# Optimization experiments

Measured on AMD Instinct MI355X. Metric: run time of the kernel, lower is better.

## Reference

```python
import jax, jax.numpy as jnp
import numpy as np

T = 8192        # total tokens
HID = 2048      # hidden_size
H = 16          # num heads
D = 128         # head_dim
INNER = H * D   # 2048
CHUNK = 128
EPS = 1e-5
SCALE = D ** -0.5
ROPE_BASE = 600000.0


def _rmsnorm(x, w, eps=EPS):
    # x: [..., d]
    var = jnp.mean(jnp.square(x), axis=-1, keepdims=True)
    return x * jax.lax.rsqrt(var + eps) * w


def _rope(x, positions):
    # neox-style rope on full head_dim. x: [T, H, D], positions: [T]
    half = D // 2
    inv_freq = 1.0 / (ROPE_BASE ** (jnp.arange(half, dtype=jnp.float32) / half))
    ang = positions.astype(jnp.float32)[:, None] * inv_freq          # [T, half]
    cos = jnp.cos(ang)[:, None, :]                                   # [T, 1, half]
    sin = jnp.sin(ang)[:, None, :]
    x1, x2 = x[..., :half], x[..., half:]
    return jnp.concatenate([x1 * cos - x2 * sin, x2 * cos + x1 * sin], axis=-1)


def setup_inputs() -> dict:
    key = jax.random.key(0)
    ks = jax.random.split(key, 5)
    hidden_states = jax.random.normal(ks[0], (T, HID), dtype=jnp.float32)
    positions = jnp.arange(T, dtype=jnp.int64 if jax.config.jax_enable_x64 else jnp.int32)
    Wqkv = jax.random.normal(ks[1], (HID, 3 * INNER), dtype=jnp.float32) * 0.02
    q_ln_w = jnp.ones((D,), dtype=jnp.float32)
    k_ln_w = jnp.ones((D,), dtype=jnp.float32)
    Wg = jax.random.normal(ks[2], (HID, INNER), dtype=jnp.float32) * 0.02
    g_norm_w = jnp.ones((INNER,), dtype=jnp.float32)
    Wo = jax.random.normal(ks[3], (INNER, HID), dtype=jnp.float32) * 0.02
    return {"hidden_states": hidden_states, "positions": positions, "Wqkv": Wqkv,
            "q_ln_w": q_ln_w, "k_ln_w": k_ln_w, "Wg": Wg,
            "g_norm_w": g_norm_w, "Wo": Wo}


def reference(hidden_states, positions, Wqkv, q_ln_w, k_ln_w, Wg, g_norm_w, Wo):
    x = hidden_states.astype(jnp.float32)
    qkv = jax.nn.silu(x @ Wqkv)                                  # linear_silu=True, fp32
    q, k, v = jnp.split(qkv, [INNER, 2 * INNER], axis=-1)
    # per-head QK RMSNorm
    q = _rmsnorm(q.reshape(T, H, D), q_ln_w)
    k = _rmsnorm(k.reshape(T, H, D), k_ln_w)
    # rope
    q = _rope(q, positions)
    k = _rope(k, positions)
    v = v.reshape(T, H, D)
    q = q * SCALE  # scaling passed to RadixAttention

    # chunked causal linear attention: o_t = q_t @ sum_{s<=t} k_s v_s^T
    N = T // CHUNK
    qc = q.reshape(N, CHUNK, H, D)
    kc = k.reshape(N, CHUNK, H, D)
    vc = v.reshape(N, CHUNK, H, D)
    mask = jnp.tril(jnp.ones((CHUNK, CHUNK), dtype=jnp.float32))  # causal within chunk

    def step(S, chunk):
        qi, ki, vi = chunk                                        # [C, H, D]
        scores = jnp.einsum('chd,shd->hcs', qi, ki) * mask        # intra-chunk causal
        o = jnp.einsum('hcs,shd->chd', scores, vi)
        o = o + jnp.einsum('chd,hde->che', qi, S)                 # inter-chunk state
        S = S + jnp.einsum('chd,che->hde', ki, vi)
        return S, o

    S0 = jnp.zeros((H, D, D), dtype=jnp.float32)
    _, o = jax.lax.scan(step, S0, (qc, kc, vc))                   # o: [N, C, H, D]
    o = o.reshape(T, INNER)

    gate = x @ Wg                                                 # g_proj
    normed = _rmsnorm(o, g_norm_w)                                # group_norm_size == 1
    gated = jax.nn.sigmoid(gate) * normed
    return gated @ Wo                                             # out proj (no bias)
```

## Files before the change

### kernel.cpp

```cpp
#include <hip/hip_runtime.h>
#include <cstdint>
#include <cstddef>

typedef unsigned short u16;
typedef __attribute__((ext_vector_type(8))) short short8;
typedef __attribute__((ext_vector_type(4))) float f32x4;

#define T_SEQ 8192
#define NH 16
#define HD 128
#define NCH 64
#define KDIM 2048

constexpr float EPS = 1e-5f;
constexpr float SCALE = 0.08838834764831845f;

__device__ __forceinline__ u16 f2bf(float f) {
  union { float f; unsigned u; } v; v.f = f;
  unsigned r = v.u + 0x7fffu + ((v.u >> 16) & 1u);
  return (u16)(r >> 16);
}
__device__ __forceinline__ float bf2f(u16 h) {
  union { unsigned u; float f; } v; v.u = ((unsigned)h) << 16;
  return v.f;
}
__device__ __forceinline__ unsigned pack2(u16 a, u16 b) {
  return (unsigned)a | ((unsigned)b << 16);
}
__device__ __forceinline__ f32x4 mfma16(short8 a, short8 b, f32x4 c) {
  return __builtin_amdgcn_mfma_f32_16x16x32_bf16(a, b, c, 0, 0, 0);
}
__device__ __forceinline__ void gl2lds(const u16* g, u16* l) {
  __builtin_amdgcn_global_load_lds(
      (const __attribute__((address_space(1))) void*)g,
      (__attribute__((address_space(3))) void*)l, 16, 0, 0);
}

__global__ __launch_bounds__(256) void cast_f32_bf16(const float* __restrict__ src,
                                                     u16* __restrict__ dst, long n) {
  long i = ((long)blockIdx.x * 256 + threadIdx.x) * 8;
  if (i >= n) return;
  float4 a = *(const float4*)(src + i);
  float4 b = *(const float4*)(src + i + 4);
  alignas(16) u16 u[8] = {f2bf(a.x), f2bf(a.y), f2bf(a.z), f2bf(a.w),
                          f2bf(b.x), f2bf(b.y), f2bf(b.z), f2bf(b.w)};
  *(int4*)(dst + i) = *(const int4*)u;
}

__global__ __launch_bounds__(256) void transpose_cast(const float* __restrict__ W,
                                                      u16* __restrict__ Wt, int K, int N) {
  __shared__ u16 tile[64][72];
  int n0 = blockIdx.x * 64, k0 = blockIdx.y * 64;
  int tx = threadIdx.x, ty = threadIdx.y;
  for (int r = ty; r < 64; r += 4)
    tile[r][tx] = f2bf(W[(size_t)(k0 + r) * N + n0 + tx]);
  __syncthreads();
  for (int r = ty; r < 64; r += 4)
    Wt[(size_t)(n0 + r) * K + k0 + tx] = tile[tx][r];
}

template <int EPI>
__global__ __launch_bounds__(512) void gemm256(const u16* __restrict__ A,
                                               const u16* __restrict__ Bt, int N,
                                               float* __restrict__ Cf,
                                               u16* __restrict__ Cb,
                                               u16* __restrict__ q_t,
                                               u16* __restrict__ k_t,
                                               u16* __restrict__ v_t) {
  __shared__ u16 lds[65536];
  const int tid  = threadIdx.x;
  const int wave = tid >> 6, lane = tid & 63;
  const int lr = lane & 15, lg = lane >> 4;
  const int wr = wave >> 2, wc = wave & 3;
  const int nx = gridDim.x;
  const int nwg = nx * gridDim.y;
  const int flat = blockIdx.y * nx + blockIdx.x;
  const int logical = (flat & 7) * (nwg >> 3) + (flat >> 3);
  const int bm = logical / nx, bn = logical % nx;
  const int sx  = (lr & 7) << 4;
  const int cu0 = ((lg * 16) ^ sx) >> 1;
  const int cu1 = ((64 + lg * 16) ^ sx) >> 1;

  const int srow  = tid >> 3;
  const int sslot = (tid & 7) ^ (srow & 7);
  const u16* gA = A  + (size_t)(bm * 256 + srow) * KDIM + sslot * 8;
  const u16* gB = Bt + (size_t)(bn * 256 + srow) * KDIM + sslot * 8;
  const int sbase = wave * 512;

  f32x4 acc[8][4];
  #pragma unroll
  for (int i = 0; i < 8; i++)
    #pragma unroll
    for (int j = 0; j < 4; j++) acc[i][j] = (f32x4){0.f, 0.f, 0.f, 0.f};

  auto STAGE = [&](int op, int buf, int half, int kt) {
    const u16* g = (op ? gB : gA) + (size_t)half * 128 * KDIM + kt * 64;
    u16* l = &lds[buf * 32768 + op * 16384 + half * 8192 + sbase];
    gl2lds(g, l);
    gl2lds(g + (size_t)64 * KDIM, l + 4096);
  };

  const int aoff = (wr * 64 + lr) * 64;
  const int boff = 16384 + (wc * 32 + lr) * 64;

  STAGE(0, 0, 0, 0); STAGE(1, 0, 0, 0); STAGE(0, 0, 1, 0); STAGE(1, 0, 1, 0);
  STAGE(0, 1, 0, 1); STAGE(1, 1, 1, 1); STAGE(0, 1, 1, 1);
  asm volatile("s_waitcnt vmcnt(6)" ::: "memory");
  __builtin_amdgcn_s_barrier();

  short8 af[4][2], b0f[2][2], b1f[2][2];
  const int NT = KDIM / 64;
  for (int t = 0; t < NT; ++t) {
    const int cur = t & 1, nxt = cur ^ 1;
    const int cb = cur * 32768;
    #pragma unroll
    for (int i = 0; i < 4; i++) {
      af[i][0] = *(const short8*)&lds[cb + aoff + i * 1024 + cu0];
      af[i][1] = *(const short8*)&lds[cb + aoff + i * 1024 + cu1];
    }
    #pragma unroll
    for (int j = 0; j < 2; j++) {
      b0f[j][0] = *(const short8*)&lds[cb + boff + j * 1024 + cu0];
      b0f[j][1] = *(const short8*)&lds[cb + boff + j * 1024 + cu1];
    }
    if (t + 1 < NT) STAGE(1, nxt, 0, t + 1);
    __builtin_amdgcn_s_barrier();
    asm volatile("s_waitcnt lgkmcnt(0)" ::: "memory");
    __builtin_amdgcn_s_setprio(1);
    #pragma unroll
    for (int i = 0; i < 4; i++)
      #pragma unroll
      for (int j = 0; j < 2; j++) {
        acc[i][j] = mfma16(af[i][0], b0f[j][0], acc[i][j]);
        acc[i][j] = mfma16(af[i][1], b0f[j][1], acc[i][j]);
      }
    __builtin_amdgcn_s_setprio(0);
    __builtin_amdgcn_s_barrier();
    #pragma unroll
    for (int j = 0; j < 2; j++) {
      b1f[j][0] = *(const short8*)&lds[cb + 8192 + boff + j * 1024 + cu0];
      b1f[j][1] = *(const short8*)&lds[cb + 8192 + boff + j * 1024 + cu1];
    }
    if (t + 2 < NT) STAGE(0, cur, 0, t + 2);
    __builtin_amdgcn_s_barrier();
    asm volatile("s_waitcnt lgkmcnt(0)" ::: "memory");
    __builtin_amdgcn_s_setprio(1);
    #pragma unroll
    for (int i = 0; i < 4; i++)
      #pragma unroll
      for (int j = 0; j < 2; j++) {
        acc[i][2 + j] = mfma16(af[i][0], b1f[j][0], acc[i][2 + j]);
        acc[i][2 + j] = mfma16(af[i][1], b1f[j][1], acc[i][2 + j]);
      }
    __builtin_amdgcn_s_setprio(0);
    __builtin_amdgcn_s_barrier();
    #pragma unroll
    for (int i = 0; i < 4; i++) {
      af[i][0] = *(const short8*)&lds[cb + 8192 + aoff + i * 1024 + cu0];
      af[i][1] = *(const short8*)&lds[cb + 8192 + aoff + i * 1024 + cu1];
    }
    if (t + 2 < NT) STAGE(1, cur, 1, t + 2);
    __builtin_amdgcn_s_barrier();
    asm volatile("s_waitcnt lgkmcnt(0)" ::: "memory");
    __builtin_amdgcn_s_setprio(1);
    #pragma unroll
    for (int i = 0; i < 4; i++)
      #pragma unroll
      for (int j = 0; j < 2; j++) {
        acc[4 + i][2 + j] = mfma16(af[i][0], b1f[j][0], acc[4 + i][2 + j]);
        acc[4 + i][2 + j] = mfma16(af[i][1], b1f[j][1], acc[4 + i][2 + j]);
      }
    __builtin_amdgcn_s_setprio(0);
    __builtin_amdgcn_s_barrier();
    if (t + 2 < NT) STAGE(0, cur, 1, t + 2);
    __builtin_amdgcn_s_barrier();
    asm volatile("s_waitcnt lgkmcnt(0)" ::: "memory");
    __builtin_amdgcn_s_setprio(1);
    #pragma unroll
    for (int i = 0; i < 4; i++)
      #pragma unroll
      for (int j = 0; j < 2; j++) {
        acc[4 + i][j] = mfma16(af[i][0], b0f[j][0], acc[4 + i][j]);
        acc[4 + i][j] = mfma16(af[i][1], b0f[j][1], acc[4 + i][j]);
      }
    __builtin_amdgcn_s_setprio(0);
    if (t + 2 < NT) asm volatile("s_waitcnt vmcnt(6)" ::: "memory");
    else            asm volatile("s_waitcnt vmcnt(0)" ::: "memory");
    __builtin_amdgcn_s_barrier();
  }

  #pragma unroll
  for (int mi = 0; mi < 8; mi++)
    #pragma unroll
    for (int nj = 0; nj < 4; nj++)
      #pragma unroll
      for (int r = 0; r < 4; r++) {
        int row = bm * 256 + (mi >> 2) * 128 + wr * 64 + (mi & 3) * 16 + lg * 4 + r;
        int col = bn * 256 + (nj >> 1) * 128 + wc * 32 + (nj & 1) * 16 + lr;
        float v = acc[mi][nj][r];
        if (EPI == 0) {
          Cf[(size_t)row * N + col] = v;
        } else if (EPI == 1) {
          Cb[(size_t)row * N + col] = f2bf(v);
        } else {
          float s = v / (1.0f + __expf(-v));
          int part = col >> 11;
          int h = (col >> 7) & 15;
          int d = col & 127;
          u16* dst = part == 0 ? q_t : (part == 1 ? k_t : v_t);
          dst[((size_t)h * T_SEQ + row) * HD + d] = f2bf(s);
        }
      }
}

__global__ __launch_bounds__(256) void qk_prep(u16* __restrict__ q_t, u16* __restrict__ k_t,
                                               const int* __restrict__ positions,
                                               const float* __restrict__ q_ln_w,
                                               const float* __restrict__ k_ln_w) {
  const int t = blockIdx.x;
  const int h = blockIdx.y * 4 + (threadIdx.x >> 6);
  const int lane = threadIdx.x & 63;
  const int d0 = lane * 2;
  const size_t base = ((size_t)h * T_SEQ + t) * HD + d0;
  unsigned qu = *(const unsigned*)(q_t + base);
  unsigned ku = *(const unsigned*)(k_t + base);
  float q0 = bf2f((u16)qu), q1 = bf2f((u16)(qu >> 16));
  float k0 = bf2f((u16)ku), k1 = bf2f((u16)(ku >> 16));
  float s1 = q0 * q0 + q1 * q1;
  float s2 = k0 * k0 + k1 * k1;
  #pragma unroll
  for (int off = 32; off > 0; off >>= 1) {
    s1 += __shfl_xor(s1, off);
    s2 += __shfl_xor(s2, off);
  }
  float rq = rsqrtf(s1 * (1.0f / 128.0f) + EPS);
  float rk = rsqrtf(s2 * (1.0f / 128.0f) + EPS);
  float w0 = q_ln_w[d0], w1 = q_ln_w[d0 + 1];
  float u0 = k_ln_w[d0], u1 = k_ln_w[d0 + 1];
  float qn0 = q0 * rq * w0, qn1 = q1 * rq * w1;
  float kn0 = k0 * rk * u0, kn1 = k1 * rk * u1;
  float qp0 = __shfl_xor(qn0, 32), qp1 = __shfl_xor(qn1, 32);
  float kp0 = __shfl_xor(kn0, 32), kp1 = __shfl_xor(kn1, 32);
  int i0 = d0 & 63;
  float invf0 = exp2f((float)i0 * (-19.194593f / 64.0f));
  float invf1 = exp2f((float)(i0 + 1) * (-19.194593f / 64.0f));
  float pos = (float)positions[t];
  float a0 = pos * invf0, a1 = pos * invf1;
  float c0 = cosf(a0), sn0 = sinf(a0), c1 = cosf(a1), sn1 = sinf(a1);
  bool lo = lane < 32;
  float qr0 = lo ? (qn0 * c0 - qp0 * sn0) : (qn0 * c0 + qp0 * sn0);
  float qr1 = lo ? (qn1 * c1 - qp1 * sn1) : (qn1 * c1 + qp1 * sn1);
  float kr0 = lo ? (kn0 * c0 - kp0 * sn0) : (kn0 * c0 + kp0 * sn0);
  float kr1 = lo ? (kn1 * c1 - kp1 * sn1) : (kn1 * c1 + kp1 * sn1);
  *(unsigned*)(q_t + base) = pack2(f2bf(qr0 * SCALE), f2bf(qr1 * SCALE));
  *(unsigned*)(k_t + base) = pack2(f2bf(kr0), f2bf(kr1));
}

__global__ __launch_bounds__(256) void attn_phaseB(const u16* __restrict__ k_t,
                                                   const u16* __restrict__ v_t,
                                                   u16* __restrict__ G) {
  const int c = blockIdx.x, h = blockIdx.y;
  __shared__ u16 lV[128 * 72];
  __shared__ u16 lK[128 * 72];
  const int tid = threadIdx.x, wave = tid >> 6, lane = tid & 63;
  const int wm = (wave >> 1) * 64, wn = (wave & 1) * 64;
  const int lr = lane & 15, lg = lane >> 4;
  f32x4 acc[4][4];
  #pragma unroll
  for (int i = 0; i < 4; i++)
    #pragma unroll
    for (int j = 0; j < 4; j++) acc[i][j] = (f32x4){0.f, 0.f, 0.f, 0.f};

  const int t0 = (tid >> 4) * 4;
  const int ds = (tid & 15) * 8;
  for (int h2 = 0; h2 < 2; h2++) {
    __syncthreads();
    const u16* vsrc = v_t + ((size_t)h * T_SEQ + c * 128 + h2 * 64 + t0) * HD + ds;
    const u16* ksrc = k_t + ((size_t)h * T_SEQ + c * 128 + h2 * 64 + t0) * HD + ds;
    int4 rv[4], rk[4];
    #pragma unroll
    for (int r = 0; r < 4; r++) {
      rv[r] = *(const int4*)(vsrc + r * HD);
      rk[r] = *(const int4*)(ksrc + r * HD);
    }
    const u16* v0 = (const u16*)&rv[0]; const u16* v1 = (const u16*)&rv[1];
    const u16* v2 = (const u16*)&rv[2]; const u16* v3 = (const u16*)&rv[3];
    const u16* K0 = (const u16*)&rk[0]; const u16* K1 = (const u16*)&rk[1];
    const u16* K2 = (const u16*)&rk[2]; const u16* K3 = (const u16*)&rk[3];
    #pragma unroll
    for (int j = 0; j < 8; j++) {
      uint2 wv, wk;
      wv.x = pack2(v0[j], v1[j]); wv.y = pack2(v2[j], v3[j]);
      wk.x = pack2(K0[j], K1[j]); wk.y = pack2(K2[j], K3[j]);
      *(uint2*)&lV[(ds + j) * 72 + t0] = wv;
      *(uint2*)&lK[(ds + j) * 72 + t0] = wk;
    }
    __syncthreads();
    #pragma unroll
    for (int kk = 0; kk < 64; kk += 32) {
      short8 af[4], bfr[4];
      #pragma unroll
      for (int i = 0; i < 4; i++)
        af[i] = *(const short8*)&lV[(wm + i * 16 + lr) * 72 + kk + lg * 8];
      #pragma unroll
      for (int j = 0; j < 4; j++)
        bfr[j] = *(const short8*)&lK[(wn + j * 16 + lr) * 72 + kk + lg * 8];
      #pragma unroll
      for (int i = 0; i < 4; i++)
        #pragma unroll
        for (int j = 0; j < 4; j++)
          acc[i][j] = mfma16(af[i], bfr[j], acc[i][j]);
    }
  }
  u16* Gp = G + ((size_t)h * NCH + c) * 16384;
  #pragma unroll
  for (int i = 0; i < 4; i++)
    #pragma unroll
    for (int j = 0; j < 4; j++)
      #pragma unroll
      for (int r = 0; r < 4; r++)
        Gp[(wm + i * 16 + lg * 4 + r) * 128 + wn + j * 16 + lr] = f2bf(acc[i][j][r]);
}

__global__ __launch_bounds__(256) void prefix_S(u16* __restrict__ G) {
  int idx = blockIdx.x * 256 + threadIdx.x;
  int h = idx >> 12;
  int e4 = (idx & 4095) * 4;
  float run0 = 0.f, run1 = 0.f, run2 = 0.f, run3 = 0.f;
  size_t base = (size_t)h * NCH * 16384 + e4;
  for (int c = 0; c < NCH; c++) {
    uint2 g = *(uint2*)&G[base + (size_t)c * 16384];
    float a0 = bf2f((u16)g.x), a1 = bf2f((u16)(g.x >> 16));
    float a2 = bf2f((u16)g.y), a3 = bf2f((u16)(g.y >> 16));
    uint2 o;
    o.x = pack2(f2bf(run0), f2bf(run1));
    o.y = pack2(f2bf(run2), f2bf(run3));
    *(uint2*)&G[base + (size_t)c * 16384] = o;
    run0 += a0; run1 += a1; run2 += a2; run3 += a3;
  }
}

__global__ __launch_bounds__(256) void attn_phaseC(const u16* __restrict__ q_t,
                                                   const u16* __restrict__ k_t,
                                                   const u16* __restrict__ v_t,
                                                   const u16* __restrict__ G,
                                                   u16* __restrict__ o_hm) {
  const int c = blockIdx.x, h = blockIdx.y;
  __shared__ u16 lP[128 * 136];
  __shared__ u16 lV[128 * 72];
  const int tid = threadIdx.x, wave = tid >> 6, lane = tid & 63;
  const int wm = wave * 32;
  const int lr = lane & 15, lg = lane >> 4;

  f32x4 acc1[2][8], acc2[2][8];
  #pragma unroll
  for (int i = 0; i < 2; i++)
    #pragma unroll
    for (int j = 0; j < 8; j++) {
      acc1[i][j] = (f32x4){0.f, 0.f, 0.f, 0.f};
      acc2[i][j] = (f32x4){0.f, 0.f, 0.f, 0.f};
    }

  const u16* Sp = G + ((size_t)h * NCH + c) * 16384;
  const u16* qbase = q_t + ((size_t)h * T_SEQ + c * 128) * HD;
  const u16* kbase = k_t + ((size_t)h * T_SEQ + c * 128) * HD;

  #pragma unroll
  for (int kk = 0; kk < 128; kk += 32) {
    short8 af[2];
    #pragma unroll
    for (int i = 0; i < 2; i++)
      af[i] = *(const short8*)(qbase + (wm + i * 16 + lr) * HD + kk + lg * 8);
    #pragma unroll
    for (int j = 0; j < 8; j++) {
      short8 bK = *(const short8*)(kbase + (j * 16 + lr) * HD + kk + lg * 8);
      short8 bS = *(const short8*)(Sp + (j * 16 + lr) * 128 + kk + lg * 8);
      #pragma unroll
      for (int i = 0; i < 2; i++) {
        acc1[i][j] = mfma16(af[i], bK, acc1[i][j]);
        acc2[i][j] = mfma16(af[i], bS, acc2[i][j]);
      }
    }
  }
  #pragma unroll
  for (int i = 0; i < 2; i++)
    #pragma unroll
    for (int j = 0; j < 8; j++)
      #pragma unroll
      for (int r = 0; r < 4; r++) {
        int row = wm + i * 16 + lg * 4 + r;
        int col = j * 16 + lr;
        float v = (col <= row) ? acc1[i][j][r] : 0.0f;
        lP[row * 136 + col] = f2bf(v);
      }

  const int t0 = (tid >> 4) * 4;
  const int ds = (tid & 15) * 8;
  for (int sh2 = 0; sh2 < 2; sh2++) {
    __syncthreads();
    const u16* vsrc = v_t + ((size_t)h * T_SEQ + c * 128 + sh2 * 64 + t0) * HD + ds;
    int4 rv[4];
    #pragma unroll
    for (int r = 0; r < 4; r++) rv[r] = *(const int4*)(vsrc + r * HD);
    const u16* v0 = (const u16*)&rv[0]; const u16* v1 = (const u16*)&rv[1];
    const u16* v2 = (const u16*)&rv[2]; const u16* v3 = (const u16*)&rv[3];
    #pragma unroll
    for (int j = 0; j < 8; j++) {
      uint2 wv;
      wv.x = pack2(v0[j], v1[j]); wv.y = pack2(v2[j], v3[j]);
      *(uint2*)&lV[(ds + j) * 72 + t0] = wv;
    }
    __syncthreads();
    #pragma unroll
    for (int kk = 0; kk < 64; kk += 32) {
      short8 af[2];
      #pragma unroll
      for (int i = 0; i < 2; i++)
        af[i] = *(const short8*)&lP[(wm + i * 16 + lr) * 136 + sh2 * 64 + kk + lg * 8];
      #pragma unroll
      for (int j = 0; j < 8; j++) {
        short8 bV = *(const short8*)&lV[(j * 16 + lr) * 72 + kk + lg * 8];
        #pragma unroll
        for (int i = 0; i < 2; i++)
          acc2[i][j] = mfma16(af[i], bV, acc2[i][j]);
      }
    }
  }
  u16* op = o_hm + ((size_t)h * NCH + c) * 16384;
  #pragma unroll
  for (int i = 0; i < 2; i++)
    #pragma unroll
    for (int j = 0; j < 8; j++)
      #pragma unroll
      for (int r = 0; r < 4; r++) {
        int row = wm + i * 16 + lg * 4 + r;
        int e = j * 16 + lr;
        op[row * 128 + e] = f2bf(acc2[i][j][r]);
      }
}

__global__ __launch_bounds__(256) void gated_kernel(const u16* __restrict__ o_hm,
                                                    const u16* __restrict__ gate_bf,
                                                    const float* __restrict__ g_norm_w,
                                                    u16* __restrict__ gated_bf) {
  const int t = blockIdx.x, tid = threadIdx.x;
  const int h = tid >> 4, e0 = (tid & 15) * 8;
  const int c = t >> 7, row = t & 127;
  short8 ov = *(const short8*)(o_hm + (((size_t)h * NCH + c) * 128 + row) * 128 + e0);
  const u16* ovp = (const u16*)&ov;
  float vals[8], ss = 0.f;
  #pragma unroll
  for (int j = 0; j < 8; j++) {
    float v = bf2f(ovp[j]);
    vals[j] = v;
    ss += v * v;
  }
  #pragma unroll
  for (int off = 32; off > 0; off >>= 1) ss += __shfl_xor(ss, off);
  __shared__ float sh[4];
  if ((tid & 63) == 0) sh[tid >> 6] = ss;
  __syncthreads();
  ss = sh[0] + sh[1] + sh[2] + sh[3];
  float r = rsqrtf(ss * (1.0f / 2048.0f) + EPS);
  short8 gv = *(const short8*)(gate_bf + (size_t)t * 2048 + tid * 8);
  const u16* gvp = (const u16*)&gv;
  float4 w0 = *(const float4*)(g_norm_w + tid * 8);
  float4 w1 = *(const float4*)(g_norm_w + tid * 8 + 4);
  float wv[8] = {w0.x, w0.y, w0.z, w0.w, w1.x, w1.y, w1.z, w1.w};
  alignas(16) u16 outu[8];
  #pragma unroll
  for (int j = 0; j < 8; j++) {
    float normed = vals[j] * r * wv[j];
    float g = bf2f(gvp[j]);
    float sg = 1.0f / (1.0f + __expf(-g));
    outu[j] = f2bf(normed * sg);
  }
  *(int4*)(gated_bf + (size_t)t * 2048 + tid * 8) = *(const int4*)outu;
}

extern "C" void kernel_launch(void* const* d_in, const int* in_sizes, int n_in,
                              void* d_out, int out_size, void* d_ws, size_t ws_size,
                              hipStream_t stream) {
  const float* x = (const float*)d_in[0];
  const int* positions = (const int*)d_in[1];
  const float* Wqkv = (const float*)d_in[2];
  const float* q_ln_w = (const float*)d_in[3];
  const float* k_ln_w = (const float*)d_in[4];
  const float* Wg = (const float*)d_in[5];
  const float* g_norm_w = (const float*)d_in[6];
  const float* Wo = (const float*)d_in[7];
  float* out = (float*)d_out;

  char* ws = (char*)d_ws;
  const size_t M32 = (size_t)32 * 1024 * 1024;
  u16* WqkvT   = (u16*)ws;
  u16* G       = (u16*)ws;
  u16* WgT     = (u16*)(ws + M32);
  u16* q_t     = (u16*)(ws + M32 + 8388608);
  u16* gated   = q_t;
  u16* k_t     = (u16*)(ws + M32 + 8388608 + M32);
  u16* gate_bf = k_t;
  u16* v_t     = (u16*)(ws + M32 + 8388608 + 2 * M32);
  u16* WoT     = v_t;
  u16* x_bf    = (u16*)(ws + M32 + 8388608 + 3 * M32);
  const size_t needed = M32 + 8388608 + 4 * M32;
  if (ws_size < needed) return;

  cast_f32_bf16<<<8192, 256, 0, stream>>>(x, x_bf, (long)8192 * 2048);
  transpose_cast<<<dim3(96, 32), dim3(64, 4), 0, stream>>>(Wqkv, WqkvT, 2048, 6144);
  transpose_cast<<<dim3(32, 32), dim3(64, 4), 0, stream>>>(Wg, WgT, 2048, 2048);

  gemm256<2><<<dim3(24, 32), 512, 0, stream>>>(x_bf, WqkvT, 6144, nullptr, nullptr, q_t, k_t, v_t);

  qk_prep<<<dim3(8192, 4), 256, 0, stream>>>(q_t, k_t, positions, q_ln_w, k_ln_w);

  attn_phaseB<<<dim3(64, 16), 256, 0, stream>>>(k_t, v_t, G);
  prefix_S<<<256, 256, 0, stream>>>(G);
  attn_phaseC<<<dim3(64, 16), 256, 0, stream>>>(q_t, k_t, v_t, G, G);

  gemm256<1><<<dim3(8, 32), 512, 0, stream>>>(x_bf, WgT, 2048, nullptr, gate_bf, nullptr, nullptr, nullptr);
  gated_kernel<<<8192, 256, 0, stream>>>(G, gate_bf, g_norm_w, gated);

  transpose_cast<<<dim3(32, 32), dim3(64, 4), 0, stream>>>(Wo, WoT, 2048, 2048);
  gemm256<0><<<dim3(8, 32), 512, 0, stream>>>(gated, WoT, 2048, out, nullptr, nullptr, nullptr, nullptr);
}
```

Baseline: 634.0 us.

## Fuse QK RMSNorm and RoPE into QKV GEMM epilogue via LDS-staged coalesced stores

The QKV GEMM epilogue now stages accumulator tiles through LDS so each wave holds full 128-wide head rows. It applies SiLU, per-head RMSNorm and RoPE in registers before writing vectorised bf16 stores, which removes the separate qk_prep kernel and its read-modify-write pass over q and k. The gate GEMM also gets the LDS-staged vectorised store path in place of scattered 2-byte stores. The prefix_S loop is manually unrolled by four so several loads are in flight at once. The costs are extra LDS round trips and barriers in the epilogue, plus more registers held live at the end of the kernel.

```diff
diff --git a/kernel.cpp b/kernel.cpp
--- a/kernel.cpp
+++ b/kernel.cpp
@@ -66,7 +66,10 @@
                                                u16* __restrict__ Cb,
                                                u16* __restrict__ q_t,
                                                u16* __restrict__ k_t,
-                                               u16* __restrict__ v_t) {
+                                               u16* __restrict__ v_t,
+                                               const int* __restrict__ positions,
+                                               const float* __restrict__ q_ln_w,
+                                               const float* __restrict__ k_ln_w) {
   __shared__ u16 lds[65536];
   const int tid  = threadIdx.x;
   const int wave = tid >> 6, lane = tid & 63;
@@ -189,71 +192,102 @@
     __builtin_amdgcn_s_barrier();
   }
 
-  #pragma unroll
-  for (int mi = 0; mi < 8; mi++)
-    #pragma unroll
-    for (int nj = 0; nj < 4; nj++)
-      #pragma unroll
-      for (int r = 0; r < 4; r++) {
-        int row = bm * 256 + (mi >> 2) * 128 + wr * 64 + (mi & 3) * 16 + lg * 4 + r;
-        int col = bn * 256 + (nj >> 1) * 128 + wc * 32 + (nj & 1) * 16 + lr;
-        float v = acc[mi][nj][r];
-        if (EPI == 0) {
-          Cf[(size_t)row * N + col] = v;
-        } else if (EPI == 1) {
-          Cb[(size_t)row * N + col] = f2bf(v);
+  if (EPI == 0) {
+    #pragma unroll
+    for (int mi = 0; mi < 8; mi++)
+      #pragma unroll
+      for (int nj = 0; nj < 4; nj++)
+        #pragma unroll
+        for (int r = 0; r < 4; r++) {
+          int row = bm * 256 + (mi >> 2) * 128 + wr * 64 + (mi & 3) * 16 + lg * 4 + r;
+          int col = bn * 256 + (nj >> 1) * 128 + wc * 32 + (nj & 1) * 16 + lr;
+          Cf[(size_t)row * N + col] = acc[mi][nj][r];
+        }
+    return;
+  }
+
+  float* lf = (float*)lds;
+  const int STR = 268;
+  #pragma unroll
+  for (int q = 0; q < 4; ++q) {
+    __builtin_amdgcn_s_barrier();
+    if (wr == (q & 1)) {
+      const int mi0 = (q >> 1) * 4;
+      #pragma unroll
+      for (int m = 0; m < 4; m++)
+        #pragma unroll
+        for (int nj = 0; nj < 4; nj++)
+          #pragma unroll
+          for (int r = 0; r < 4; r++) {
+            int rl = m * 16 + lg * 4 + r;
+            int cl = wc * 32 + (nj >> 1) * 128 + (nj & 1) * 16 + lr;
+            lf[rl * STR + cl] = acc[mi0 + m][nj][r];
+          }
+    }
+    __builtin_amdgcn_s_barrier();
+    for (int s = 0; s < 8; ++s) {
+      const int rl = s * 8 + wave;
+      const int trow = bm * 256 + q * 64 + rl;
+      const float* rp = &lf[rl * STR + lane * 4];
+      float v0 = rp[0], v1 = rp[1], v2 = rp[2], v3 = rp[3];
+      if (EPI == 3) {
+        unsigned lo = pack2(f2bf(v0), f2bf(v1));
+        unsigned hi = pack2(f2bf(v2), f2bf(v3));
+        uint2 o; o.x = lo; o.y = hi;
+        *(uint2*)&Cb[(size_t)trow * 2048 + bn * 256 + lane * 4] = o;
+      } else {
+        float x0 = v0 / (1.0f + __expf(-v0));
+        float x1 = v1 / (1.0f + __expf(-v1));
+        float x2 = v2 / (1.0f + __expf(-v2));
+        float x3 = v3 / (1.0f + __expf(-v3));
+        const int col = bn * 256 + lane * 4;
+        const int h = (col >> 7) & 15;
+        const int d0 = (lane & 31) * 4;
+        if (bn < 16) {
+          float ss = x0 * x0 + x1 * x1 + x2 * x2 + x3 * x3;
+          ss += __shfl_xor(ss, 1);
+          ss += __shfl_xor(ss, 2);
+          ss += __shfl_xor(ss, 4);
+          ss += __shfl_xor(ss, 8);
+          ss += __shfl_xor(ss, 16);
+          float rn = rsqrtf(ss * (1.0f / 128.0f) + EPS);
+          const float* wp = (bn < 8) ? q_ln_w : k_ln_w;
+          float4 w = *(const float4*)(wp + d0);
+          float n0 = x0 * rn * w.x, n1 = x1 * rn * w.y;
+          float n2 = x2 * rn * w.z, n3 = x3 * rn * w.w;
+          float p0 = __shfl_xor(n0, 16), p1 = __shfl_xor(n1, 16);
+          float p2 = __shfl_xor(n2, 16), p3 = __shfl_xor(n3, 16);
+          const int i0 = d0 & 63;
+          const float pos = (float)positions[trow];
+          float a0 = pos * exp2f((float)(i0 + 0) * (-19.194593f / 64.0f));
+          float a1 = pos * exp2f((float)(i0 + 1) * (-19.194593f / 64.0f));
+          float a2 = pos * exp2f((float)(i0 + 2) * (-19.194593f / 64.0f));
+          float a3 = pos * exp2f((float)(i0 + 3) * (-19.194593f / 64.0f));
+          float c0 = cosf(a0), s0 = sinf(a0);
+          float c1 = cosf(a1), s1 = sinf(a1);
+          float c2 = cosf(a2), s2 = sinf(a2);
+          float c3 = cosf(a3), s3 = sinf(a3);
+          const bool hi = (lane & 16) != 0;
+          float o0 = hi ? (n0 * c0 + p0 * s0) : (n0 * c0 - p0 * s0);
+          float o1 = hi ? (n1 * c1 + p1 * s1) : (n1 * c1 - p1 * s1);
+          float o2 = hi ? (n2 * c2 + p2 * s2) : (n2 * c2 - p2 * s2);
+          float o3 = hi ? (n3 * c3 + p3 * s3) : (n3 * c3 - p3 * s3);
+          u16* dst;
+          if (bn < 8) {
+            o0 *= SCALE; o1 *= SCALE; o2 *= SCALE; o3 *= SCALE;
+            dst = q_t;
+          } else {
+            dst = k_t;
+          }
+          uint2 o; o.x = pack2(f2bf(o0), f2bf(o1)); o.y = pack2(f2bf(o2), f2bf(o3));
+          *(uint2*)&dst[((size_t)h * T_SEQ + trow) * HD + d0] = o;
         } else {
-          float s = v / (1.0f + __expf(-v));
-          int part = col >> 11;
-          int h = (col >> 7) & 15;
-          int d = col & 127;
-          u16* dst = part == 0 ? q_t : (part == 1 ? k_t : v_t);
-          dst[((size_t)h * T_SEQ + row) * HD + d] = f2bf(s);
+          uint2 o; o.x = pack2(f2bf(x0), f2bf(x1)); o.y = pack2(f2bf(x2), f2bf(x3));
+          *(uint2*)&v_t[((size_t)h * T_SEQ + trow) * HD + d0] = o;
         }
       }
-}
-
-__global__ __launch_bounds__(256) void qk_prep(u16* __restrict__ q_t, u16* __restrict__ k_t,
-                                               const int* __restrict__ positions,
-                                               const float* __restrict__ q_ln_w,
-                                               const float* __restrict__ k_ln_w) {
-  const int t = blockIdx.x;
-  const int h = blockIdx.y * 4 + (threadIdx.x >> 6);
-  const int lane = threadIdx.x & 63;
-  const int d0 = lane * 2;
-  const size_t base = ((size_t)h * T_SEQ + t) * HD + d0;
-  unsigned qu = *(const unsigned*)(q_t + base);
-  unsigned ku = *(const unsigned*)(k_t + base);
-  float q0 = bf2f((u16)qu), q1 = bf2f((u16)(qu >> 16));
-  float k0 = bf2f((u16)ku), k1 = bf2f((u16)(ku >> 16));
-  float s1 = q0 * q0 + q1 * q1;
-  float s2 = k0 * k0 + k1 * k1;
-  #pragma unroll
-  for (int off = 32; off > 0; off >>= 1) {
-    s1 += __shfl_xor(s1, off);
-    s2 += __shfl_xor(s2, off);
-  }
-  float rq = rsqrtf(s1 * (1.0f / 128.0f) + EPS);
-  float rk = rsqrtf(s2 * (1.0f / 128.0f) + EPS);
-  float w0 = q_ln_w[d0], w1 = q_ln_w[d0 + 1];
-  float u0 = k_ln_w[d0], u1 = k_ln_w[d0 + 1];
-  float qn0 = q0 * rq * w0, qn1 = q1 * rq * w1;
-  float kn0 = k0 * rk * u0, kn1 = k1 * rk * u1;
-  float qp0 = __shfl_xor(qn0, 32), qp1 = __shfl_xor(qn1, 32);
-  float kp0 = __shfl_xor(kn0, 32), kp1 = __shfl_xor(kn1, 32);
-  int i0 = d0 & 63;
-  float invf0 = exp2f((float)i0 * (-19.194593f / 64.0f));
-  float invf1 = exp2f((float)(i0 + 1) * (-19.194593f / 64.0f));
-  float pos = (float)positions[t];
-  float a0 = pos * invf0, a1 = pos * invf1;
-  float c0 = cosf(a0), sn0 = sinf(a0), c1 = cosf(a1), sn1 = sinf(a1);
-  bool lo = lane < 32;
-  float qr0 = lo ? (qn0 * c0 - qp0 * sn0) : (qn0 * c0 + qp0 * sn0);
-  float qr1 = lo ? (qn1 * c1 - qp1 * sn1) : (qn1 * c1 + qp1 * sn1);
-  float kr0 = lo ? (kn0 * c0 - kp0 * sn0) : (kn0 * c0 + kp0 * sn0);
-  float kr1 = lo ? (kn1 * c1 - kp1 * sn1) : (kn1 * c1 + kp1 * sn1);
-  *(unsigned*)(q_t + base) = pack2(f2bf(qr0 * SCALE), f2bf(qr1 * SCALE));
-  *(unsigned*)(k_t + base) = pack2(f2bf(kr0), f2bf(kr1));
+    }
+  }
 }
 
 __global__ __launch_bounds__(256) void attn_phaseB(const u16* __restrict__ k_t,
@@ -326,17 +360,30 @@
   int idx = blockIdx.x * 256 + threadIdx.x;
   int h = idx >> 12;
   int e4 = (idx & 4095) * 4;
-  float run0 = 0.f, run1 = 0.f, run2 = 0.f, run3 = 0.f;
+  float r0 = 0.f, r1 = 0.f, r2 = 0.f, r3 = 0.f;
   size_t base = (size_t)h * NCH * 16384 + e4;
-  for (int c = 0; c < NCH; c++) {
-    uint2 g = *(uint2*)&G[base + (size_t)c * 16384];
-    float a0 = bf2f((u16)g.x), a1 = bf2f((u16)(g.x >> 16));
-    float a2 = bf2f((u16)g.y), a3 = bf2f((u16)(g.y >> 16));
+  for (int c = 0; c < NCH; c += 4) {
+    uint2 g0 = *(uint2*)&G[base + (size_t)(c + 0) * 16384];
+    uint2 g1 = *(uint2*)&G[base + (size_t)(c + 1) * 16384];
+    uint2 g2 = *(uint2*)&G[base + (size_t)(c + 2) * 16384];
+    uint2 g3 = *(uint2*)&G[base + (size_t)(c + 3) * 16384];
     uint2 o;
-    o.x = pack2(f2bf(run0), f2bf(run1));
-    o.y = pack2(f2bf(run2), f2bf(run3));
-    *(uint2*)&G[base + (size_t)c * 16384] = o;
-    run0 += a0; run1 += a1; run2 += a2; run3 += a3;
+    o.x = pack2(f2bf(r0), f2bf(r1)); o.y = pack2(f2bf(r2), f2bf(r3));
+    *(uint2*)&G[base + (size_t)(c + 0) * 16384] = o;
+    r0 += bf2f((u16)g0.x); r1 += bf2f((u16)(g0.x >> 16));
+    r2 += bf2f((u16)g0.y); r3 += bf2f((u16)(g0.y >> 16));
+    o.x = pack2(f2bf(r0), f2bf(r1)); o.y = pack2(f2bf(r2), f2bf(r3));
+    *(uint2*)&G[base + (size_t)(c + 1) * 16384] = o;
+    r0 += bf2f((u16)g1.x); r1 += bf2f((u16)(g1.x >> 16));
+    r2 += bf2f((u16)g1.y); r3 += bf2f((u16)(g1.y >> 16));
+    o.x = pack2(f2bf(r0), f2bf(r1)); o.y = pack2(f2bf(r2), f2bf(r3));
+    *(uint2*)&G[base + (size_t)(c + 2) * 16384] = o;
+    r0 += bf2f((u16)g2.x); r1 += bf2f((u16)(g2.x >> 16));
+    r2 += bf2f((u16)g2.y); r3 += bf2f((u16)(g2.y >> 16));
+    o.x = pack2(f2bf(r0), f2bf(r1)); o.y = pack2(f2bf(r2), f2bf(r3));
+    *(uint2*)&G[base + (size_t)(c + 3) * 16384] = o;
+    r0 += bf2f((u16)g3.x); r1 += bf2f((u16)(g3.x >> 16));
+    r2 += bf2f((u16)g3.y); r3 += bf2f((u16)(g3.y >> 16));
   }
 }
 
@@ -510,17 +557,18 @@
   transpose_cast<<<dim3(96, 32), dim3(64, 4), 0, stream>>>(Wqkv, WqkvT, 2048, 6144);
   transpose_cast<<<dim3(32, 32), dim3(64, 4), 0, stream>>>(Wg, WgT, 2048, 2048);
 
-  gemm256<2><<<dim3(24, 32), 512, 0, stream>>>(x_bf, WqkvT, 6144, nullptr, nullptr, q_t, k_t, v_t);
-
-  qk_prep<<<dim3(8192, 4), 256, 0, stream>>>(q_t, k_t, positions, q_ln_w, k_ln_w);
+  gemm256<2><<<dim3(24, 32), 512, 0, stream>>>(x_bf, WqkvT, 6144, nullptr, nullptr,
+                                               q_t, k_t, v_t, positions, q_ln_w, k_ln_w);
 
   attn_phaseB<<<dim3(64, 16), 256, 0, stream>>>(k_t, v_t, G);
   prefix_S<<<256, 256, 0, stream>>>(G);
   attn_phaseC<<<dim3(64, 16), 256, 0, stream>>>(q_t, k_t, v_t, G, G);
 
-  gemm256<1><<<dim3(8, 32), 512, 0, stream>>>(x_bf, WgT, 2048, nullptr, gate_bf, nullptr, nullptr, nullptr);
+  gemm256<3><<<dim3(8, 32), 512, 0, stream>>>(x_bf, WgT, 2048, nullptr, gate_bf,
+                                              nullptr, nullptr, nullptr, nullptr, nullptr, nullptr);
   gated_kernel<<<8192, 256, 0, stream>>>(G, gate_bf, g_norm_w, gated);
 
   transpose_cast<<<dim3(32, 32), dim3(64, 4), 0, stream>>>(Wo, WoT, 2048, 2048);
-  gemm256<0><<<dim3(8, 32), 512, 0, stream>>>(gated, WoT, 2048, out, nullptr, nullptr, nullptr, nullptr);
-}
+  gemm256<0><<<dim3(8, 32), 512, 0, stream>>>(gated, WoT, 2048, out, nullptr,
+                                              nullptr, nullptr, nullptr, nullptr, nullptr, nullptr);
+}
```

Result: slower. 700.9 us (+10.5%).
